# Kernel tuning notes

Hardware: AMD Instinct MI355X
Metric: run time of the kernel (lower is better)

## Reference

```python
import math
import jax, jax.numpy as jnp
import numpy as np

D = 4  # BWGNN d


def calculate_theta2(d):
    # Faithful numeric reimplementation of the sympy version.
    # f_i(x) = (x/2)^i (1-x/2)^(d-i) / (2*Beta(i+1, d+1-i)); the original code
    # keeps only the d lowest-order (ascending) coefficients, dropping x^d.
    thetas = []
    for i in range(d):
        c1 = np.zeros(i + 1); c1[i] = 0.5 ** i                      # (x/2)^i
        c2 = np.array([math.comb(d - i, j) * (-0.5) ** j
                       for j in range(d - i + 1)])                   # (1-x/2)^(d-i)
        c = np.convolve(c1, c2)                                      # ascending, len d+1
        B = math.factorial(i) * math.factorial(d - i) / math.factorial(d + 1)
        c = c / (2.0 * B)
        thetas.append([float(c[j]) for j in range(d)])               # coeff[d-i] slicing
    return thetas

THETAS = calculate_theta2(D)


def setup_inputs() -> dict:
    key = jax.random.key(0)
    k1, k2, k3, k4 = jax.random.split(key, 4)
    N, E, F_in, H = 100000, 1600000, 128, 64
    feature = jax.random.normal(k1, (N, F_in), dtype=jnp.float32)
    edge_index = jax.random.randint(k2, (2, E), 0, N, dtype=jnp.int32)
    W = jax.random.normal(k3, (F_in, H), dtype=jnp.float32) * 0.05
    b = jax.random.normal(k4, (H,), dtype=jnp.float32) * 0.05
    return {"feature": feature, "edge_index": edge_index, "W": W, "b": b}


def reference(feature, edge_index, W, b):
    N = feature.shape[0]
    src, dst = edge_index[0], edge_index[1]
    # out_degrees: number of out-edges per node (src side), clamped to >= 1
    deg = jax.ops.segment_sum(jnp.ones_like(src, dtype=jnp.float32), src,
                              num_segments=N)
    D_invsqrt = jnp.maximum(deg, 1.0) ** -0.5  # [N]
    D_invsqrt = D_invsqrt[:, None]             # [N,1]

    h = jax.nn.leaky_relu(feature @ W + b, negative_slope=0.01)  # [N,H]

    def unn_laplacian(feat):
        # feat - D^{-1/2} A^T D^{-1/2} feat  (copy_u + sum over dst)
        msg = (feat * D_invsqrt)[src]                          # [E,H]
        agg = jax.ops.segment_sum(msg, dst, num_segments=N)    # [N,H]
        return feat - agg * D_invsqrt

    outs = []
    for theta in THETAS:
        feat = h
        acc = theta[0] * feat
        for k in range(1, len(theta)):
            feat = unn_laplacian(feat)
            acc = acc + theta[k] * feat
        outs.append(acc)
    return jnp.concatenate(outs, axis=1)  # [N, len(THETAS)*H]
```

## Files before the change

kernel.cpp:

```cpp
#include <hip/hip_runtime.h>

#define THREADS 256
#define T1 4096
#define BCAP 8192
#define NBMAX 512

__device__ __forceinline__ float bf2f(unsigned short u) {
    return __uint_as_float(((unsigned int)u) << 16);
}
__device__ __forceinline__ unsigned short f2bf(float x) {
    unsigned int u = __float_as_uint(x);
    u += 0x7fffu + ((u >> 16) & 1u);
    return (unsigned short)(u >> 16);
}
__device__ __forceinline__ float blo(unsigned int x) { return __uint_as_float(x << 16); }
__device__ __forceinline__ float bhi(unsigned int x) { return __uint_as_float(x & 0xffff0000u); }

__global__ void zero_kernel(int* __restrict__ p, int n) {
    const int i = blockIdx.x * blockDim.x + threadIdx.x;
    if (i < n) p[i] = 0;
}

__global__ void bin_kernel(const int* __restrict__ src, const int* __restrict__ dst,
                           int* __restrict__ gFillD, unsigned int* __restrict__ gBufD,
                           int* __restrict__ gFillS, unsigned int* __restrict__ gBufS,
                           int E, int tiles) {
    __shared__ int cnt[NBMAX], scanB[NBMAX], gbase[NBMAX], place[NBMAX];
    __shared__ unsigned int stage[T1], addr[T1];
    const int tid = threadIdx.x;
    const bool isS = blockIdx.x >= tiles;
    const int tile = isS ? blockIdx.x - tiles : blockIdx.x;
    const int* key = isS ? src : dst;
    int* gFill = isS ? gFillS : gFillD;
    unsigned int* gBuf = isS ? gBufS : gBufD;
    const int tileStart = tile * T1;
    const int tileCnt = min(T1, E - tileStart);

    for (int i = tid; i < NBMAX; i += THREADS) { cnt[i] = 0; place[i] = 0; }
    __syncthreads();

    for (int i = tid; i < tileCnt; i += THREADS)
        atomicAdd(&cnt[key[tileStart + i] >> 8], 1);
    __syncthreads();

    if (tid < 64) {
        const int base = tid * 8;
        int loc[8]; int s = 0;
        #pragma unroll
        for (int k = 0; k < 8; ++k) { loc[k] = s; s += cnt[base + k]; }
        int run = s;
        #pragma unroll
        for (int off = 1; off < 64; off <<= 1) {
            int t = __shfl_up(run, off);
            if (tid >= off) run += t;
        }
        const int excl = run - s;
        #pragma unroll
        for (int k = 0; k < 8; ++k) scanB[base + k] = excl + loc[k];
    }
    __syncthreads();

    for (int i = tid; i < NBMAX; i += THREADS)
        gbase[i] = atomicAdd(&gFill[i], cnt[i]);
    __syncthreads();

    for (int i = tid; i < tileCnt; i += THREADS) {
        const int kk = key[tileStart + i];
        const int b = kk >> 8;
        const unsigned int rec = isS ? (unsigned int)(kk & 255)
                                     : (((unsigned int)(kk & 255) << 17) | (unsigned int)src[tileStart + i]);
        const int pos = atomicAdd(&place[b], 1);
        const int li = scanB[b] + pos;
        const int gi = gbase[b] + pos;
        stage[li] = rec;
        addr[li] = (gi < BCAP) ? (unsigned int)(b * BCAP + gi) : 0xFFFFFFFFu;
    }
    __syncthreads();

    for (int i = tid; i < tileCnt; i += THREADS) {
        const unsigned int a = addr[i];
        if (a != 0xFFFFFFFFu) gBuf[a] = stage[i];
    }
}

__global__ void scanb_kernel(const int* __restrict__ gFill, int* __restrict__ gBase,
                             int* __restrict__ rowptr, int nb, int N) {
    __shared__ int s[NBMAX];
    const int tid = threadIdx.x;
    const int v = (tid < nb) ? min(gFill[tid], BCAP) : 0;
    s[tid] = v;
    __syncthreads();
    for (int off = 1; off < NBMAX; off <<= 1) {
        int t = (tid >= off) ? s[tid - off] : 0;
        __syncthreads();
        s[tid] += t;
        __syncthreads();
    }
    if (tid < nb) gBase[tid] = s[tid] - v;
    if (tid == NBMAX - 1) rowptr[N] = s[NBMAX - 1];
}

__global__ void csr_kernel(const int* __restrict__ gFillD, const int* __restrict__ gBase,
                           const unsigned int* __restrict__ gBufD,
                           const int* __restrict__ gFillS, const unsigned int* __restrict__ gBufS,
                           int* __restrict__ rowptr, int* __restrict__ col,
                           int* __restrict__ deg, int N) {
    __shared__ int fillT[256], offT[256], place[256], sc[256];
    __shared__ int colT[BCAP];
    __shared__ int nwrite;
    const int tid = threadIdx.x;
    const int b = blockIdx.x;
    const int nrec = min(gFillD[b], BCAP);
    const int base = gBase[b];

    fillT[tid] = 0; place[tid] = 0;
    __syncthreads();
    for (int i = tid; i < nrec; i += THREADS)
        atomicAdd(&fillT[gBufD[(size_t)b * BCAP + i] >> 17], 1);
    __syncthreads();

    int v = fillT[tid];
    sc[tid] = v;
    __syncthreads();
    for (int off = 1; off < 256; off <<= 1) {
        int t = (tid >= off) ? sc[tid - off] : 0;
        __syncthreads();
        sc[tid] += t;
        __syncthreads();
    }
    offT[tid] = sc[tid] - v;
    if (tid == 255) nwrite = sc[255];
    __syncthreads();

    const int node0 = b << 8;
    const int nvalid = min(256, N - node0);
    if (tid < nvalid) rowptr[node0 + tid] = base + offT[tid];

    for (int i = tid; i < nrec; i += THREADS) {
        const unsigned int rec = gBufD[(size_t)b * BCAP + i];
        const int dlow = rec >> 17;
        const int s = rec & 0x1FFFF;
        const int pos = atomicAdd(&place[dlow], 1);
        colT[offT[dlow] + pos] = s;
    }
    __syncthreads();

    const int nw = nwrite;
    for (int i = tid; i < nw; i += THREADS) col[base + i] = colT[i];

    fillT[tid] = 0;
    __syncthreads();
    const int nrecS = min(gFillS[b], BCAP);
    for (int i = tid; i < nrecS; i += THREADS)
        atomicAdd(&fillT[gBufS[(size_t)b * BCAP + i] & 255], 1);
    __syncthreads();
    if (tid < nvalid) deg[node0 + tid] = fillT[tid];
}

__global__ void count_fb(const int* __restrict__ src, const int* __restrict__ dst,
                         int* __restrict__ deg, int* __restrict__ cntd, int E) {
    const int stride = gridDim.x * blockDim.x;
    for (int i = blockIdx.x * blockDim.x + threadIdx.x; i < E; i += stride) {
        atomicAdd(&deg[src[i]], 1);
        atomicAdd(&cntd[dst[i]], 1);
    }
}
__global__ void scan_fb(const int* __restrict__ cnt, int* __restrict__ rowptr, int N) {
    __shared__ int s[256];
    __shared__ int carry;
    const int tid = threadIdx.x;
    if (tid == 0) carry = 0;
    __syncthreads();
    for (int basei = 0; basei < N; basei += 256) {
        const int i = basei + tid;
        const int v = (i < N) ? cnt[i] : 0;
        s[tid] = v;
        __syncthreads();
        for (int off = 1; off < 256; off <<= 1) {
            int t = (tid >= off) ? s[tid - off] : 0;
            __syncthreads();
            s[tid] += t;
            __syncthreads();
        }
        if (i < N) rowptr[i] = carry + s[tid] - v;
        __syncthreads();
        if (tid == 0) carry += s[255];
        __syncthreads();
    }
    if (tid == 0) rowptr[N] = carry;
}
__global__ void fill_fb(const int* __restrict__ src, const int* __restrict__ dst,
                        const int* __restrict__ rowptr, int* __restrict__ place,
                        int* __restrict__ col, int E) {
    const int stride = gridDim.x * blockDim.x;
    for (int i = blockIdx.x * blockDim.x + threadIdx.x; i < E; i += stride) {
        const int d = dst[i];
        col[rowptr[d] + atomicAdd(&place[d], 1)] = src[i];
    }
}

__global__ void gemm_leaky(const float* __restrict__ feat, const float* __restrict__ W,
                           const float* __restrict__ b, const int* __restrict__ deg,
                           unsigned short* __restrict__ S0, int N) {
    __shared__ float Wl[128 * 64];
    __shared__ float fl_t[128][65];
    __shared__ float bl[64];

    {
        const float4* W4 = (const float4*)W;
        float4* Wl4 = (float4*)Wl;
        for (int i = threadIdx.x; i < 2048; i += THREADS) Wl4[i] = W4[i];
        if (threadIdx.x < 64) bl[threadIdx.x] = b[threadIdx.x];
    }

    const int cg = threadIdx.x & 15;
    const int rg = threadIdx.x >> 4;
    const int ntiles = (N + 63) >> 6;

    for (int tile = blockIdx.x; tile < ntiles; tile += gridDim.x) {
        const int n0 = tile << 6;
        __syncthreads();
        for (int i = threadIdx.x; i < 2048; i += THREADS) {
            const int rr = i >> 5;
            const int kk = i & 31;
            float4 v = make_float4(0.f, 0.f, 0.f, 0.f);
            if (n0 + rr < N) v = ((const float4*)(feat + (size_t)(n0 + rr) * 128))[kk];
            fl_t[kk * 4 + 0][rr] = v.x;
            fl_t[kk * 4 + 1][rr] = v.y;
            fl_t[kk * 4 + 2][rr] = v.z;
            fl_t[kk * 4 + 3][rr] = v.w;
        }
        __syncthreads();

        float acc[4][4];
        #pragma unroll
        for (int j = 0; j < 4; ++j) {
            float bv = bl[cg * 4 + j];
            acc[0][j] = bv; acc[1][j] = bv; acc[2][j] = bv; acc[3][j] = bv;
        }

        #pragma unroll 4
        for (int k = 0; k < 128; ++k) {
            const float4 w = *((const float4*)&Wl[k * 64 + cg * 4]);
            const float4 f = *((const float4*)&fl_t[k][rg * 4]);
            acc[0][0] += f.x * w.x; acc[0][1] += f.x * w.y; acc[0][2] += f.x * w.z; acc[0][3] += f.x * w.w;
            acc[1][0] += f.y * w.x; acc[1][1] += f.y * w.y; acc[1][2] += f.y * w.z; acc[1][3] += f.y * w.w;
            acc[2][0] += f.z * w.x; acc[2][1] += f.z * w.y; acc[2][2] += f.z * w.z; acc[2][3] += f.z * w.w;
            acc[3][0] += f.w * w.x; acc[3][1] += f.w * w.y; acc[3][2] += f.w * w.z; acc[3][3] += f.w * w.w;
        }

        #pragma unroll
        for (int i = 0; i < 4; ++i) {
            const int n = n0 + rg * 4 + i;
            if (n < N) {
                const float dv = rsqrtf(fmaxf((float)deg[n], 1.0f));
                ushort4 o;
                float v0 = acc[i][0] > 0.f ? acc[i][0] : 0.01f * acc[i][0];
                float v1 = acc[i][1] > 0.f ? acc[i][1] : 0.01f * acc[i][1];
                float v2 = acc[i][2] > 0.f ? acc[i][2] : 0.01f * acc[i][2];
                float v3 = acc[i][3] > 0.f ? acc[i][3] : 0.01f * acc[i][3];
                o.x = f2bf(v0 * dv); o.y = f2bf(v1 * dv); o.z = f2bf(v2 * dv); o.w = f2bf(v3 * dv);
                *((ushort4*)(S0 + (size_t)n * 64 + cg * 4)) = o;
            }
        }
    }
}

template<bool FINAL>
__global__ void hop_kernel(const int* __restrict__ rowptr, const int* __restrict__ col,
                           const int* __restrict__ deg,
                           const unsigned short* __restrict__ Sprev,
                           unsigned short* __restrict__ Snext,
                           const unsigned short* __restrict__ S0,
                           const unsigned short* __restrict__ S1,
                           float* __restrict__ out, int N) {
    const int lane = threadIdx.x & 63;
    const int g = lane >> 3;
    const int q = lane & 7;
    const int nwaves = (gridDim.x * blockDim.x) >> 6;
    for (int n = (blockIdx.x * blockDim.x + threadIdx.x) >> 6; n < N; n += nwaves) {
        const int beg = rowptr[n];
        const int end = rowptr[n + 1];
        float a[8];
        #pragma unroll
        for (int k = 0; k < 8; ++k) a[k] = 0.f;

        for (int e0 = beg; e0 < end; e0 += 64) {
            const int idx = e0 + lane;
            const int c = (idx < end) ? col[idx] : 0;
            const int m = min(64, end - e0);
            for (int j = 0; j < m; j += 16) {
                const int jg0 = j + g;
                const int jg1 = j + 8 + g;
                const int s0 = __shfl(c, jg0 & 63);
                const int s1 = __shfl(c, jg1 & 63);
                const bool v0 = jg0 < m;
                const bool v1 = jg1 < m;
                uint4 u0, u1;
                if (v0) u0 = *(const uint4*)(Sprev + (size_t)s0 * 64 + q * 8);
                if (v1) u1 = *(const uint4*)(Sprev + (size_t)s1 * 64 + q * 8);
                if (v0) {
                    a[0] += blo(u0.x); a[1] += bhi(u0.x);
                    a[2] += blo(u0.y); a[3] += bhi(u0.y);
                    a[4] += blo(u0.z); a[5] += bhi(u0.z);
                    a[6] += blo(u0.w); a[7] += bhi(u0.w);
                }
                if (v1) {
                    a[0] += blo(u1.x); a[1] += bhi(u1.x);
                    a[2] += blo(u1.y); a[3] += bhi(u1.y);
                    a[4] += blo(u1.z); a[5] += bhi(u1.z);
                    a[6] += blo(u1.w); a[7] += bhi(u1.w);
                }
            }
        }
        #pragma unroll
        for (int k = 0; k < 8; ++k) {
            a[k] += __shfl_xor(a[k], 8);
            a[k] += __shfl_xor(a[k], 16);
            a[k] += __shfl_xor(a[k], 32);
        }

        const float d = fmaxf((float)deg[n], 1.0f);
        const float inv = 1.0f / d;
        const uint4 uo = *(const uint4*)(Sprev + (size_t)n * 64 + q * 8);
        float own[8], sn[8];
        own[0] = blo(uo.x); own[1] = bhi(uo.x); own[2] = blo(uo.y); own[3] = bhi(uo.y);
        own[4] = blo(uo.z); own[5] = bhi(uo.z); own[6] = blo(uo.w); own[7] = bhi(uo.w);
        #pragma unroll
        for (int k = 0; k < 8; ++k) sn[k] = own[k] - a[k] * inv;

        if (!FINAL) {
            if (g == 0) {
                uint4 w;
                w.x = (unsigned int)f2bf(sn[0]) | ((unsigned int)f2bf(sn[1]) << 16);
                w.y = (unsigned int)f2bf(sn[2]) | ((unsigned int)f2bf(sn[3]) << 16);
                w.z = (unsigned int)f2bf(sn[4]) | ((unsigned int)f2bf(sn[5]) << 16);
                w.w = (unsigned int)f2bf(sn[6]) | ((unsigned int)f2bf(sn[7]) << 16);
                *((uint4*)(Snext + (size_t)n * 64 + q * 8)) = w;
            }
        } else if (g < 4) {
            const float sc = sqrtf(d);
            const uint4 u0 = *(const uint4*)(S0 + (size_t)n * 64 + q * 8);
            const uint4 u1 = *(const uint4*)(S1 + (size_t)n * 64 + q * 8);
            float h[8], p1[8];
            h[0] = blo(u0.x); h[1] = bhi(u0.x); h[2] = blo(u0.y); h[3] = bhi(u0.y);
            h[4] = blo(u0.z); h[5] = bhi(u0.z); h[6] = blo(u0.w); h[7] = bhi(u0.w);
            p1[0] = blo(u1.x); p1[1] = bhi(u1.x); p1[2] = blo(u1.y); p1[3] = bhi(u1.y);
            p1[4] = blo(u1.z); p1[5] = bhi(u1.z); p1[6] = blo(u1.w); p1[7] = bhi(u1.w);
            float c0, c1, c2, c3;
            if (g == 0)      { c0 = 2.5f; c1 = -5.0f; c2 = 3.75f;  c3 = -1.25f; }
            else if (g == 1) { c0 = 0.f;  c1 = 5.0f;  c2 = -7.5f;  c3 = 3.75f;  }
            else if (g == 2) { c0 = 0.f;  c1 = 0.f;   c2 = 3.75f;  c3 = -3.75f; }
            else             { c0 = 0.f;  c1 = 0.f;   c2 = 0.f;    c3 = 1.25f;  }
            float o[8];
            #pragma unroll
            for (int k = 0; k < 8; ++k) {
                const float hv = h[k] * sc, p1v = p1[k] * sc, p2v = own[k] * sc, p3v = sn[k] * sc;
                o[k] = c0 * hv + c1 * p1v + c2 * p2v + c3 * p3v;
            }
            float* op = out + (size_t)n * 256 + g * 64 + q * 8;
            *((float4*)op)       = make_float4(o[0], o[1], o[2], o[3]);
            *((float4*)(op + 4)) = make_float4(o[4], o[5], o[6], o[7]);
        }
    }
}

extern "C" void kernel_launch(void* const* d_in, const int* in_sizes, int n_in,
                              void* d_out, int out_size, void* d_ws, size_t ws_size,
                              hipStream_t stream) {
    const float* feature = (const float*)d_in[0];
    const int*   eidx    = (const int*)d_in[1];
    const float* W       = (const float*)d_in[2];
    const float* b       = (const float*)d_in[3];
    float* out = (float*)d_out;

    const int N = in_sizes[0] / 128;
    const int E = in_sizes[1] / 2;
    const int* src = eidx;
    const int* dst = eidx + E;

    const int nb = (N + 255) >> 8;

    int* deg    = (int*)d_ws;
    int* fill   = deg + N;
    int* rowptr = fill + N;
    int* col    = rowptr + (N + 1);
    int* gFillD = col + E;
    int* gFillS = gFillD + NBMAX;
    int* gBase  = gFillS + NBMAX;
    unsigned int* gBufD = (unsigned int*)(gBase + NBMAX);
    unsigned int* gBufS = gBufD + (size_t)nb * BCAP;
    unsigned short* S0 = (unsigned short*)(((uintptr_t)(gBufS + (size_t)nb * BCAP) + 255) & ~(uintptr_t)255);
    unsigned short* S1 = S0 + (size_t)N * 64;
    unsigned short* S2 = S1 + (size_t)N * 64;

    if (N <= 131072) {
        zero_kernel<<<(2 * NBMAX + THREADS - 1) / THREADS, THREADS, 0, stream>>>(gFillD, 2 * NBMAX);
        const int tiles = (E + T1 - 1) / T1;
        bin_kernel<<<2 * tiles, THREADS, 0, stream>>>(src, dst, gFillD, gBufD, gFillS, gBufS, E, tiles);
        scanb_kernel<<<1, NBMAX, 0, stream>>>(gFillD, gBase, rowptr, nb, N);
        csr_kernel<<<nb, THREADS, 0, stream>>>(gFillD, gBase, gBufD, gFillS, gBufS, rowptr, col, deg, N);
    } else {
        zero_kernel<<<(2 * N + THREADS - 1) / THREADS, THREADS, 0, stream>>>(deg, 2 * N);
        count_fb<<<2048, THREADS, 0, stream>>>(src, dst, deg, fill, E);
        scan_fb<<<1, 256, 0, stream>>>(fill, rowptr, N);
        zero_kernel<<<(N + THREADS - 1) / THREADS, THREADS, 0, stream>>>(fill, N);
        fill_fb<<<2048, THREADS, 0, stream>>>(src, dst, rowptr, fill, col, E);
    }

    const int gemm_blocks = (N + 63) / 64;
    gemm_leaky<<<gemm_blocks, THREADS, 0, stream>>>(feature, W, b, deg, S0, N);

    const int gblocks = (N + 3) / 4;
    hop_kernel<false><<<gblocks, THREADS, 0, stream>>>(rowptr, col, deg, S0, S1, S0, S0, out, N);
    hop_kernel<false><<<gblocks, THREADS, 0, stream>>>(rowptr, col, deg, S1, S2, S0, S0, out, N);
    hop_kernel<true ><<<gblocks, THREADS, 0, stream>>>(rowptr, col, deg, S2, S2, S0, S1, out, N);
}
```

Before: 234.2 us.

## Process two nodes per wavefront in hop kernels and fold block scan into CSR

The hop kernels now give each wavefront two nodes (n and n+half). When both have at most 32 in-edges, all gathers for both are issued up front, which raises memory-level parallelism and halves the number of waves. Nodes with more edges fall back to the old per-node routine. Separately, the single-block bucket scan kernel is removed and every csr_kernel block recomputes the prefix over bucket fills with wave shuffles, saving one launch at the cost of redundant scan work. More registers per thread may lower occupancy.

Measured after the change: 247.2 us. 1.06x slower.

```diff
diff --git a/kernel.cpp b/kernel.cpp
--- a/kernel.cpp
+++ b/kernel.cpp
@@ -83,35 +83,39 @@
     }
 }
 
-__global__ void scanb_kernel(const int* __restrict__ gFill, int* __restrict__ gBase,
-                             int* __restrict__ rowptr, int nb, int N) {
-    __shared__ int s[NBMAX];
-    const int tid = threadIdx.x;
-    const int v = (tid < nb) ? min(gFill[tid], BCAP) : 0;
-    s[tid] = v;
-    __syncthreads();
-    for (int off = 1; off < NBMAX; off <<= 1) {
-        int t = (tid >= off) ? s[tid - off] : 0;
-        __syncthreads();
-        s[tid] += t;
-        __syncthreads();
-    }
-    if (tid < nb) gBase[tid] = s[tid] - v;
-    if (tid == NBMAX - 1) rowptr[N] = s[NBMAX - 1];
-}
-
-__global__ void csr_kernel(const int* __restrict__ gFillD, const int* __restrict__ gBase,
-                           const unsigned int* __restrict__ gBufD,
+__global__ void csr_kernel(const int* __restrict__ gFillD, const unsigned int* __restrict__ gBufD,
                            const int* __restrict__ gFillS, const unsigned int* __restrict__ gBufS,
                            int* __restrict__ rowptr, int* __restrict__ col,
-                           int* __restrict__ deg, int N) {
+                           int* __restrict__ deg, int N, int nb) {
+    __shared__ int sg[NBMAX], scanG[NBMAX];
     __shared__ int fillT[256], offT[256], place[256], sc[256];
     __shared__ int colT[BCAP];
     __shared__ int nwrite;
     const int tid = threadIdx.x;
     const int b = blockIdx.x;
-    const int nrec = min(gFillD[b], BCAP);
-    const int base = gBase[b];
+
+    for (int i = tid; i < NBMAX; i += THREADS) sg[i] = (i < nb) ? min(gFillD[i], BCAP) : 0;
+    __syncthreads();
+    if (tid < 64) {
+        const int base = tid * 8;
+        int loc[8]; int s = 0;
+        #pragma unroll
+        for (int k = 0; k < 8; ++k) { loc[k] = s; s += sg[base + k]; }
+        int run = s;
+        #pragma unroll
+        for (int off = 1; off < 64; off <<= 1) {
+            int t = __shfl_up(run, off);
+            if (tid >= off) run += t;
+        }
+        const int excl = run - s;
+        #pragma unroll
+        for (int k = 0; k < 8; ++k) scanG[base + k] = excl + loc[k];
+    }
+    __syncthreads();
+
+    const int nrec = sg[b];
+    const int base = scanG[b];
+    if (b == 0 && tid == 0) rowptr[N] = scanG[NBMAX - 1] + sg[NBMAX - 1];
 
     fillT[tid] = 0; place[tid] = 0;
     __syncthreads();
@@ -267,6 +271,99 @@
 }
 
 template<bool FINAL>
+__device__ void hop_one(int n, const int* __restrict__ rowptr, const int* __restrict__ col,
+                        const int* __restrict__ deg,
+                        const unsigned short* __restrict__ Sprev,
+                        unsigned short* __restrict__ Snext,
+                        const unsigned short* __restrict__ S0,
+                        const unsigned short* __restrict__ S1,
+                        float* __restrict__ out, int lane, int g, int q) {
+    const int beg = rowptr[n];
+    const int end = rowptr[n + 1];
+    float a[8];
+    #pragma unroll
+    for (int k = 0; k < 8; ++k) a[k] = 0.f;
+
+    for (int e0 = beg; e0 < end; e0 += 64) {
+        const int idx = e0 + lane;
+        const int c = (idx < end) ? col[idx] : 0;
+        const int m = min(64, end - e0);
+        for (int j = 0; j < m; j += 16) {
+            const int jg0 = j + g;
+            const int jg1 = j + 8 + g;
+            const int s0 = __shfl(c, jg0 & 63);
+            const int s1 = __shfl(c, jg1 & 63);
+            const bool v0 = jg0 < m;
+            const bool v1 = jg1 < m;
+            uint4 u0, u1;
+            if (v0) u0 = *(const uint4*)(Sprev + (size_t)s0 * 64 + q * 8);
+            if (v1) u1 = *(const uint4*)(Sprev + (size_t)s1 * 64 + q * 8);
+            if (v0) {
+                a[0] += blo(u0.x); a[1] += bhi(u0.x);
+                a[2] += blo(u0.y); a[3] += bhi(u0.y);
+                a[4] += blo(u0.z); a[5] += bhi(u0.z);
+                a[6] += blo(u0.w); a[7] += bhi(u0.w);
+            }
+            if (v1) {
+                a[0] += blo(u1.x); a[1] += bhi(u1.x);
+                a[2] += blo(u1.y); a[3] += bhi(u1.y);
+                a[4] += blo(u1.z); a[5] += bhi(u1.z);
+                a[6] += blo(u1.w); a[7] += bhi(u1.w);
+            }
+        }
+    }
+    #pragma unroll
+    for (int k = 0; k < 8; ++k) {
+        a[k] += __shfl_xor(a[k], 8);
+        a[k] += __shfl_xor(a[k], 16);
+        a[k] += __shfl_xor(a[k], 32);
+    }
+
+    const float d = fmaxf((float)deg[n], 1.0f);
+    const float inv = 1.0f / d;
+    const uint4 uo = *(const uint4*)(Sprev + (size_t)n * 64 + q * 8);
+    float own[8], sn[8];
+    own[0] = blo(uo.x); own[1] = bhi(uo.x); own[2] = blo(uo.y); own[3] = bhi(uo.y);
+    own[4] = blo(uo.z); own[5] = bhi(uo.z); own[6] = blo(uo.w); own[7] = bhi(uo.w);
+    #pragma unroll
+    for (int k = 0; k < 8; ++k) sn[k] = own[k] - a[k] * inv;
+
+    if (!FINAL) {
+        if (g == 0) {
+            uint4 w;
+            w.x = (unsigned int)f2bf(sn[0]) | ((unsigned int)f2bf(sn[1]) << 16);
+            w.y = (unsigned int)f2bf(sn[2]) | ((unsigned int)f2bf(sn[3]) << 16);
+            w.z = (unsigned int)f2bf(sn[4]) | ((unsigned int)f2bf(sn[5]) << 16);
+            w.w = (unsigned int)f2bf(sn[6]) | ((unsigned int)f2bf(sn[7]) << 16);
+            *((uint4*)(Snext + (size_t)n * 64 + q * 8)) = w;
+        }
+    } else if (g < 4) {
+        const float sc = sqrtf(d);
+        const uint4 u0 = *(const uint4*)(S0 + (size_t)n * 64 + q * 8);
+        const uint4 u1 = *(const uint4*)(S1 + (size_t)n * 64 + q * 8);
+        float h[8], p1[8];
+        h[0] = blo(u0.x); h[1] = bhi(u0.x); h[2] = blo(u0.y); h[3] = bhi(u0.y);
+        h[4] = blo(u0.z); h[5] = bhi(u0.z); h[6] = blo(u0.w); h[7] = bhi(u0.w);
+        p1[0] = blo(u1.x); p1[1] = bhi(u1.x); p1[2] = blo(u1.y); p1[3] = bhi(u1.y);
+        p1[4] = blo(u1.z); p1[5] = bhi(u1.z); p1[6] = blo(u1.w); p1[7] = bhi(u1.w);
+        float c0, c1, c2, c3;
+        if (g == 0)      { c0 = 2.5f; c1 = -5.0f; c2 = 3.75f;  c3 = -1.25f; }
+        else if (g == 1) { c0 = 0.f;  c1 = 5.0f;  c2 = -7.5f;  c3 = 3.75f;  }
+        else if (g == 2) { c0 = 0.f;  c1 = 0.f;   c2 = 3.75f;  c3 = -3.75f; }
+        else             { c0 = 0.f;  c1 = 0.f;   c2 = 0.f;    c3 = 1.25f;  }
+        float o[8];
+        #pragma unroll
+        for (int k = 0; k < 8; ++k) {
+            const float hv = h[k] * sc, p1v = p1[k] * sc, p2v = own[k] * sc, p3v = sn[k] * sc;
+            o[k] = c0 * hv + c1 * p1v + c2 * p2v + c3 * p3v;
+        }
+        float* op = out + (size_t)n * 256 + g * 64 + q * 8;
+        *((float4*)op)       = make_float4(o[0], o[1], o[2], o[3]);
+        *((float4*)(op + 4)) = make_float4(o[4], o[5], o[6], o[7]);
+    }
+}
+
+template<bool FINAL>
 __global__ void hop_kernel(const int* __restrict__ rowptr, const int* __restrict__ col,
                            const int* __restrict__ deg,
                            const unsigned short* __restrict__ Sprev,
@@ -277,90 +374,133 @@
     const int lane = threadIdx.x & 63;
     const int g = lane >> 3;
     const int q = lane & 7;
+    const int half = (N + 1) >> 1;
     const int nwaves = (gridDim.x * blockDim.x) >> 6;
-    for (int n = (blockIdx.x * blockDim.x + threadIdx.x) >> 6; n < N; n += nwaves) {
-        const int beg = rowptr[n];
-        const int end = rowptr[n + 1];
-        float a[8];
-        #pragma unroll
-        for (int k = 0; k < 8; ++k) a[k] = 0.f;
-
-        for (int e0 = beg; e0 < end; e0 += 64) {
-            const int idx = e0 + lane;
-            const int c = (idx < end) ? col[idx] : 0;
-            const int m = min(64, end - e0);
-            for (int j = 0; j < m; j += 16) {
-                const int jg0 = j + g;
-                const int jg1 = j + 8 + g;
-                const int s0 = __shfl(c, jg0 & 63);
-                const int s1 = __shfl(c, jg1 & 63);
-                const bool v0 = jg0 < m;
-                const bool v1 = jg1 < m;
-                uint4 u0, u1;
-                if (v0) u0 = *(const uint4*)(Sprev + (size_t)s0 * 64 + q * 8);
-                if (v1) u1 = *(const uint4*)(Sprev + (size_t)s1 * 64 + q * 8);
-                if (v0) {
-                    a[0] += blo(u0.x); a[1] += bhi(u0.x);
-                    a[2] += blo(u0.y); a[3] += bhi(u0.y);
-                    a[4] += blo(u0.z); a[5] += bhi(u0.z);
-                    a[6] += blo(u0.w); a[7] += bhi(u0.w);
+    for (int n = (blockIdx.x * blockDim.x + threadIdx.x) >> 6; n < half; n += nwaves) {
+        const int nA = n;
+        const int nB = n + half;
+        const bool hasB = nB < N;
+        const int begA = rowptr[nA];
+        const int endA = rowptr[nA + 1];
+        int begB = 0, endB = 0;
+        if (hasB) { begB = rowptr[nB]; endB = rowptr[nB + 1]; }
+        const int mA = endA - begA;
+        const int mB = endB - begB;
+
+        if (mA <= 32 && mB <= 32) {
+            const bool isA = lane < 32;
+            const int li = isA ? lane : lane - 32;
+            const int cm = isA ? mA : mB;
+            const int cbeg = isA ? begA : begB;
+            const int c = (li < cm) ? col[cbeg + li] : 0;
+
+            uint4 uA[4], uB[4];
+            bool vA[4], vB[4];
+            #pragma unroll
+            for (int k = 0; k < 4; ++k) {
+                const int r = k * 8 + g;
+                vA[k] = r < mA;
+                const int s = __shfl(c, r & 31);
+                if (vA[k]) uA[k] = *(const uint4*)(Sprev + (size_t)s * 64 + q * 8);
+            }
+            #pragma unroll
+            for (int k = 0; k < 4; ++k) {
+                const int r = k * 8 + g;
+                vB[k] = r < mB;
+                const int s = __shfl(c, 32 + (r & 31));
+                if (vB[k]) uB[k] = *(const uint4*)(Sprev + (size_t)s * 64 + q * 8);
+            }
+
+            float aA[8], aB[8];
+            #pragma unroll
+            for (int k = 0; k < 8; ++k) { aA[k] = 0.f; aB[k] = 0.f; }
+            #pragma unroll
+            for (int k = 0; k < 4; ++k) {
+                if (vA[k]) {
+                    aA[0] += blo(uA[k].x); aA[1] += bhi(uA[k].x);
+                    aA[2] += blo(uA[k].y); aA[3] += bhi(uA[k].y);
+                    aA[4] += blo(uA[k].z); aA[5] += bhi(uA[k].z);
+                    aA[6] += blo(uA[k].w); aA[7] += bhi(uA[k].w);
                 }
-                if (v1) {
-                    a[0] += blo(u1.x); a[1] += bhi(u1.x);
-                    a[2] += blo(u1.y); a[3] += bhi(u1.y);
-                    a[4] += blo(u1.z); a[5] += bhi(u1.z);
-                    a[6] += blo(u1.w); a[7] += bhi(u1.w);
+                if (vB[k]) {
+                    aB[0] += blo(uB[k].x); aB[1] += bhi(uB[k].x);
+                    aB[2] += blo(uB[k].y); aB[3] += bhi(uB[k].y);
+                    aB[4] += blo(uB[k].z); aB[5] += bhi(uB[k].z);
+                    aB[6] += blo(uB[k].w); aB[7] += bhi(uB[k].w);
                 }
             }
-        }
-        #pragma unroll
-        for (int k = 0; k < 8; ++k) {
-            a[k] += __shfl_xor(a[k], 8);
-            a[k] += __shfl_xor(a[k], 16);
-            a[k] += __shfl_xor(a[k], 32);
-        }
-
-        const float d = fmaxf((float)deg[n], 1.0f);
-        const float inv = 1.0f / d;
-        const uint4 uo = *(const uint4*)(Sprev + (size_t)n * 64 + q * 8);
-        float own[8], sn[8];
-        own[0] = blo(uo.x); own[1] = bhi(uo.x); own[2] = blo(uo.y); own[3] = bhi(uo.y);
-        own[4] = blo(uo.z); own[5] = bhi(uo.z); own[6] = blo(uo.w); own[7] = bhi(uo.w);
-        #pragma unroll
-        for (int k = 0; k < 8; ++k) sn[k] = own[k] - a[k] * inv;
-
-        if (!FINAL) {
-            if (g == 0) {
-                uint4 w;
-                w.x = (unsigned int)f2bf(sn[0]) | ((unsigned int)f2bf(sn[1]) << 16);
-                w.y = (unsigned int)f2bf(sn[2]) | ((unsigned int)f2bf(sn[3]) << 16);
-                w.z = (unsigned int)f2bf(sn[4]) | ((unsigned int)f2bf(sn[5]) << 16);
-                w.w = (unsigned int)f2bf(sn[6]) | ((unsigned int)f2bf(sn[7]) << 16);
-                *((uint4*)(Snext + (size_t)n * 64 + q * 8)) = w;
-            }
-        } else if (g < 4) {
-            const float sc = sqrtf(d);
-            const uint4 u0 = *(const uint4*)(S0 + (size_t)n * 64 + q * 8);
-            const uint4 u1 = *(const uint4*)(S1 + (size_t)n * 64 + q * 8);
-            float h[8], p1[8];
-            h[0] = blo(u0.x); h[1] = bhi(u0.x); h[2] = blo(u0.y); h[3] = bhi(u0.y);
-            h[4] = blo(u0.z); h[5] = bhi(u0.z); h[6] = blo(u0.w); h[7] = bhi(u0.w);
-            p1[0] = blo(u1.x); p1[1] = bhi(u1.x); p1[2] = blo(u1.y); p1[3] = bhi(u1.y);
-            p1[4] = blo(u1.z); p1[5] = bhi(u1.z); p1[6] = blo(u1.w); p1[7] = bhi(u1.w);
-            float c0, c1, c2, c3;
-            if (g == 0)      { c0 = 2.5f; c1 = -5.0f; c2 = 3.75f;  c3 = -1.25f; }
-            else if (g == 1) { c0 = 0.f;  c1 = 5.0f;  c2 = -7.5f;  c3 = 3.75f;  }
-            else if (g == 2) { c0 = 0.f;  c1 = 0.f;   c2 = 3.75f;  c3 = -3.75f; }
-            else             { c0 = 0.f;  c1 = 0.f;   c2 = 0.f;    c3 = 1.25f;  }
-            float o[8];
             #pragma unroll
             for (int k = 0; k < 8; ++k) {
-                const float hv = h[k] * sc, p1v = p1[k] * sc, p2v = own[k] * sc, p3v = sn[k] * sc;
-                o[k] = c0 * hv + c1 * p1v + c2 * p2v + c3 * p3v;
-            }
-            float* op = out + (size_t)n * 256 + g * 64 + q * 8;
-            *((float4*)op)       = make_float4(o[0], o[1], o[2], o[3]);
-            *((float4*)(op + 4)) = make_float4(o[4], o[5], o[6], o[7]);
+                aA[k] += __shfl_xor(aA[k], 8);
+                aA[k] += __shfl_xor(aA[k], 16);
+                aA[k] += __shfl_xor(aA[k], 32);
+                aB[k] += __shfl_xor(aB[k], 8);
+                aB[k] += __shfl_xor(aB[k], 16);
+                aB[k] += __shfl_xor(aB[k], 32);
+            }
+
+            if (!FINAL) {
+                const bool wr = (g == 0) || (g == 1 && hasB);
+                if (wr) {
+                    const int node = (g == 0) ? nA : nB;
+                    const float d = fmaxf((float)deg[node], 1.0f);
+                    const float inv = 1.0f / d;
+                    const uint4 uo = *(const uint4*)(Sprev + (size_t)node * 64 + q * 8);
+                    float own[8], sn[8];
+                    own[0] = blo(uo.x); own[1] = bhi(uo.x); own[2] = blo(uo.y); own[3] = bhi(uo.y);
+                    own[4] = blo(uo.z); own[5] = bhi(uo.z); own[6] = blo(uo.w); own[7] = bhi(uo.w);
+                    #pragma unroll
+                    for (int k = 0; k < 8; ++k) {
+                        const float av = (g == 0) ? aA[k] : aB[k];
+                        sn[k] = own[k] - av * inv;
+                    }
+                    uint4 w;
+                    w.x = (unsigned int)f2bf(sn[0]) | ((unsigned int)f2bf(sn[1]) << 16);
+                    w.y = (unsigned int)f2bf(sn[2]) | ((unsigned int)f2bf(sn[3]) << 16);
+                    w.z = (unsigned int)f2bf(sn[4]) | ((unsigned int)f2bf(sn[5]) << 16);
+                    w.w = (unsigned int)f2bf(sn[6]) | ((unsigned int)f2bf(sn[7]) << 16);
+                    *((uint4*)(Snext + (size_t)node * 64 + q * 8)) = w;
+                }
+            } else {
+                const bool wr = (g < 4) || hasB;
+                if (wr) {
+                    const int node = (g < 4) ? nA : nB;
+                    const int gb = g & 3;
+                    const float d = fmaxf((float)deg[node], 1.0f);
+                    const float inv = 1.0f / d;
+                    const float sc = sqrtf(d);
+                    const uint4 uo = *(const uint4*)(Sprev + (size_t)node * 64 + q * 8);
+                    const uint4 u0 = *(const uint4*)(S0 + (size_t)node * 64 + q * 8);
+                    const uint4 u1 = *(const uint4*)(S1 + (size_t)node * 64 + q * 8);
+                    float own[8], h[8], p1[8];
+                    own[0] = blo(uo.x); own[1] = bhi(uo.x); own[2] = blo(uo.y); own[3] = bhi(uo.y);
+                    own[4] = blo(uo.z); own[5] = bhi(uo.z); own[6] = blo(uo.w); own[7] = bhi(uo.w);
+                    h[0] = blo(u0.x); h[1] = bhi(u0.x); h[2] = blo(u0.y); h[3] = bhi(u0.y);
+                    h[4] = blo(u0.z); h[5] = bhi(u0.z); h[6] = blo(u0.w); h[7] = bhi(u0.w);
+                    p1[0] = blo(u1.x); p1[1] = bhi(u1.x); p1[2] = blo(u1.y); p1[3] = bhi(u1.y);
+                    p1[4] = blo(u1.z); p1[5] = bhi(u1.z); p1[6] = blo(u1.w); p1[7] = bhi(u1.w);
+                    float c0, c1, c2, c3;
+                    if (gb == 0)      { c0 = 2.5f; c1 = -5.0f; c2 = 3.75f;  c3 = -1.25f; }
+                    else if (gb == 1) { c0 = 0.f;  c1 = 5.0f;  c2 = -7.5f;  c3 = 3.75f;  }
+                    else if (gb == 2) { c0 = 0.f;  c1 = 0.f;   c2 = 3.75f;  c3 = -3.75f; }
+                    else              { c0 = 0.f;  c1 = 0.f;   c2 = 0.f;    c3 = 1.25f;  }
+                    float o[8];
+                    #pragma unroll
+                    for (int k = 0; k < 8; ++k) {
+                        const float av = (g < 4) ? aA[k] : aB[k];
+                        const float snv = own[k] - av * inv;
+                        const float hv = h[k] * sc, p1v = p1[k] * sc;
+                        const float p2v = own[k] * sc, p3v = snv * sc;
+                        o[k] = c0 * hv + c1 * p1v + c2 * p2v + c3 * p3v;
+                    }
+                    float* op = out + (size_t)node * 256 + gb * 64 + q * 8;
+                    *((float4*)op)       = make_float4(o[0], o[1], o[2], o[3]);
+                    *((float4*)(op + 4)) = make_float4(o[4], o[5], o[6], o[7]);
+                }
+            }
+        } else {
+            hop_one<FINAL>(nA, rowptr, col, deg, Sprev, Snext, S0, S1, out, lane, g, q);
+            if (hasB) hop_one<FINAL>(nB, rowptr, col, deg, Sprev, Snext, S0, S1, out, lane, g, q);
         }
     }
 }
@@ -387,8 +527,7 @@
     int* col    = rowptr + (N + 1);
     int* gFillD = col + E;
     int* gFillS = gFillD + NBMAX;
-    int* gBase  = gFillS + NBMAX;
-    unsigned int* gBufD = (unsigned int*)(gBase + NBMAX);
+    unsigned int* gBufD = (unsigned int*)(gFillS + NBMAX);
     unsigned int* gBufS = gBufD + (size_t)nb * BCAP;
     unsigned short* S0 = (unsigned short*)(((uintptr_t)(gBufS + (size_t)nb * BCAP) + 255) & ~(uintptr_t)255);
     unsigned short* S1 = S0 + (size_t)N * 64;
@@ -398,8 +537,7 @@
         zero_kernel<<<(2 * NBMAX + THREADS - 1) / THREADS, THREADS, 0, stream>>>(gFillD, 2 * NBMAX);
         const int tiles = (E + T1 - 1) / T1;
         bin_kernel<<<2 * tiles, THREADS, 0, stream>>>(src, dst, gFillD, gBufD, gFillS, gBufS, E, tiles);
-        scanb_kernel<<<1, NBMAX, 0, stream>>>(gFillD, gBase, rowptr, nb, N);
-        csr_kernel<<<nb, THREADS, 0, stream>>>(gFillD, gBase, gBufD, gFillS, gBufS, rowptr, col, deg, N);
+        csr_kernel<<<nb, THREADS, 0, stream>>>(gFillD, gBufD, gFillS, gBufS, rowptr, col, deg, N, nb);
     } else {
         zero_kernel<<<(2 * N + THREADS - 1) / THREADS, THREADS, 0, stream>>>(deg, 2 * N);
         count_fb<<<2048, THREADS, 0, stream>>>(src, dst, deg, fill, E);
@@ -411,7 +549,8 @@
     const int gemm_blocks = (N + 63) / 64;
     gemm_leaky<<<gemm_blocks, THREADS, 0, stream>>>(feature, W, b, deg, S0, N);
 
-    const int gblocks = (N + 3) / 4;
+    const int half = (N + 1) >> 1;
+    const int gblocks = (half + 3) / 4;
     hop_kernel<false><<<gblocks, THREADS, 0, stream>>>(rowptr, col, deg, S0, S1, S0, S0, out, N);
     hop_kernel<false><<<gblocks, THREADS, 0, stream>>>(rowptr, col, deg, S1, S2, S0, S0, out, N);
     hop_kernel<true ><<<gblocks, THREADS, 0, stream>>>(rowptr, col, deg, S2, S2, S0, S1, out, N);
```
